# Kernel optimization log

Measured on AMD Instinct MI355X. Metric: run time of the kernel, lower is better.

## Reference

```python
import jax, jax.numpy as jnp
import numpy as np

N_NODES = 100000
N_EDGES = 1600000
N_GRAPHS = 64
D_IN = 128
D_HID = 128
D_OUT = 4
LEAKY_SLOPE = 0.01  # nn.LeakyReLU default


def setup_inputs() -> dict:
    key = jax.random.key(0)
    k1, k2, k3, k4, k5 = jax.random.split(key, 5)
    x = jax.random.normal(k1, (N_NODES, D_IN), dtype=jnp.float32)
    edge_index = jax.random.randint(k2, (2, N_EDGES), 0, N_NODES, dtype=jnp.int32)
    batch = jnp.sort(jax.random.randint(k3, (N_NODES,), 0, N_GRAPHS, dtype=jnp.int32))
    s1 = 1.0 / np.sqrt(D_IN)
    W1 = jax.random.uniform(k4, (D_IN, D_HID), jnp.float32, -s1, s1)
    b1 = jnp.zeros((D_HID,), jnp.float32)
    W2 = jax.random.uniform(k5, (D_HID, D_OUT), jnp.float32, -s1, s1)
    b2 = jnp.zeros((D_OUT,), jnp.float32)
    return {"x": x, "edge_index": edge_index, "batch": batch,
            "W1": W1, "b1": b1, "W2": W2, "b2": b2}


def _gcn_conv(x, src, dst, norm, W, b, n_nodes):
    # h = X W; messages = norm * h[src]; aggregate at dst; add bias
    h = x @ W
    msg = h[src] * norm[:, None]
    agg = jax.ops.segment_sum(msg, dst, num_segments=n_nodes)
    return agg + b


def reference(x, edge_index, batch, W1, b1, W2, b2):
    n = x.shape[0]
    # add self-loops (PyG GCNConv default)
    loops = jnp.arange(n, dtype=edge_index.dtype)
    src = jnp.concatenate([edge_index[0], loops])
    dst = jnp.concatenate([edge_index[1], loops])
    # symmetric normalization: deg over target index, weight 1
    deg = jax.ops.segment_sum(jnp.ones_like(src, dtype=x.dtype), dst, num_segments=n)
    deg_is = jnp.where(deg > 0, jax.lax.rsqrt(deg), 0.0)
    norm = deg_is[src] * deg_is[dst]

    h = _gcn_conv(x, src, dst, norm, W1, b1, n)
    h = jnp.where(h >= 0, h, LEAKY_SLOPE * h)  # LeakyReLU
    # dropout is identity at inference
    h = _gcn_conv(h, src, dst, norm, W2, b2, n)

    # global mean pool over graphs
    sums = jax.ops.segment_sum(h, batch, num_segments=N_GRAPHS)
    cnts = jax.ops.segment_sum(jnp.ones((n,), h.dtype), batch, num_segments=N_GRAPHS)
    pooled = sums / jnp.maximum(cnts, 1.0)[:, None]
    return jax.nn.softmax(pooled, axis=1)
```

## Files before the change

kernel.cpp:

```cpp
#include <hip/hip_runtime.h>

#define D 128
#define NG 64
#define NPB 256
#define MAXBK 512
#define CAPB 8192
#define PCHUNK 4096
#define PLCAP 5376
#define ENTCAP 21
#define NPASS 4
#define LDA 136

typedef unsigned int uint;
typedef unsigned short ushort_t;
typedef unsigned char uchar_t;
typedef float v2f __attribute__((ext_vector_type(2)));
typedef short s8v __attribute__((ext_vector_type(8)));
typedef float f4v __attribute__((ext_vector_type(4)));

__device__ __forceinline__ uint bfr(float x) {
    uint u = __float_as_uint(x);
    return (u + 0x7FFFu + ((u >> 16) & 1u)) >> 16;
}

__global__ __launch_bounds__(256) void k_init(const float* __restrict__ W,
                                              short* __restrict__ W1T,
                                              int* __restrict__ gcur, int NBK) {
    int idx = blockIdx.x * 256 + threadIdx.x;
    int nn = idx >> 7, kk = idx & 127;
    W1T[idx] = (short)bfr(W[kk * D + nn]);
    if (idx < NBK) gcur[idx] = idx * CAPB;
}

__global__ __launch_bounds__(256) void k_part(const int* __restrict__ edge,
                                              int* __restrict__ gcur, int* __restrict__ p1,
                                              int E, int NBK) {
    __shared__ int hist[MAXBK], scn[MAXBK], curb[MAXBK], fixb[MAXBK];
    __shared__ int ps[256];
    __shared__ int sortb[PCHUNK];
    __shared__ ushort_t sbkt[PCHUNK];
    int tid = threadIdx.x;
    for (int i = tid; i < MAXBK; i += 256) { hist[i] = 0; curb[i] = 0; }
    __syncthreads();
    int lo = blockIdx.x * PCHUNK;
    int hi = min(lo + PCHUNK, E);
    int cnt = hi - lo;
    for (int e = lo + tid; e < hi; e += 256) atomicAdd(&hist[edge[E + e] >> 8], 1);
    __syncthreads();
    int a = hist[2 * tid], b = hist[2 * tid + 1];
    ps[tid] = a + b;
    __syncthreads();
    for (int o = 1; o < 256; o <<= 1) {
        int x = (tid >= o) ? ps[tid - o] : 0;
        __syncthreads();
        ps[tid] += x;
        __syncthreads();
    }
    int pe = ps[tid] - (a + b);
    scn[2 * tid] = pe;
    scn[2 * tid + 1] = pe + a;
    __syncthreads();
    for (int bk = tid; bk < NBK; bk += 256)
        if (hist[bk]) fixb[bk] = atomicAdd(&gcur[bk], hist[bk]) - scn[bk];
    __syncthreads();
    for (int e = lo + tid; e < hi; e += 256) {
        int s = edge[e];
        int d2 = edge[E + e];
        int bk = d2 >> 8;
        int r = scn[bk] + atomicAdd(&curb[bk], 1);
        sortb[r] = ((d2 & 255) << 17) | s;
        sbkt[r] = (ushort_t)bk;
    }
    __syncthreads();
    for (int p = tid; p < cnt; p += 256) {
        int bk = sbkt[p];
        p1[fixb[bk] + p] = sortb[p];
    }
}

__global__ __launch_bounds__(256) void k_place(const int* __restrict__ p1,
                                               const int* __restrict__ gcur,
                                               int* __restrict__ ed, int2* __restrict__ offdeg,
                                               float* __restrict__ dinv, int n) {
    __shared__ int cnts[256], scn[256], cur[256];
    __shared__ int outb[PLCAP];
    int tid = threadIdx.x;
    int b = blockIdx.x;
    int base = b * CAPB;
    int cnt = gcur[b] - base;
    int end = base + cnt;
    int node0 = b << 8;
    cnts[tid] = 0;
    cur[tid] = 0;
    __syncthreads();
    int ent[ENTCAP];
    int ne = 0;
    for (int p = base + tid; p < end; p += 256) {
        int v = p1[p];
        if (ne < ENTCAP) ent[ne] = v;
        ne++;
        atomicAdd(&cnts[v >> 17], 1);
    }
    __syncthreads();
    int v0 = cnts[tid];
    scn[tid] = v0;
    __syncthreads();
    for (int o = 1; o < 256; o <<= 1) {
        int x = (tid >= o) ? scn[tid - o] : 0;
        __syncthreads();
        scn[tid] += x;
        __syncthreads();
    }
    int excl = scn[tid] - v0;
    int node = node0 + tid;
    if (node < n) {
        offdeg[node] = make_int2(base + excl, v0);
        dinv[node] = rsqrtf((float)(v0 + 1));
    }
    scn[tid] = excl;
    __syncthreads();
    int m = (ne < ENTCAP) ? ne : ENTCAP;
    for (int k = 0; k < m; ++k) {
        int v = ent[k];
        int l = v >> 17;
        int r = scn[l] + atomicAdd(&cur[l], 1);
        if (r < PLCAP) outb[r] = v & 0x1FFFF;
        else ed[base + r] = v & 0x1FFFF;
    }
    for (int p = base + tid + ENTCAP * 256; p < end; p += 256) {
        int v = p1[p];
        int l = v >> 17;
        int r = scn[l] + atomicAdd(&cur[l], 1);
        if (r < PLCAP) outb[r] = v & 0x1FFFF;
        else ed[base + r] = v & 0x1FFFF;
    }
    __syncthreads();
    int lim = (cnt < PLCAP) ? cnt : PLCAP;
    for (int p = tid; p < lim; p += 256) ed[base + p] = outb[p];
}

__global__ __launch_bounds__(256) void k_gemm_mfma(const float* __restrict__ X,
                                                   const short* __restrict__ W1T,
                                                   const float* __restrict__ dinv,
                                                   uchar_t* __restrict__ H8b, int M) {
    __shared__ short sA[128 * LDA];
    __shared__ short sB[128 * LDA];
    __shared__ float sDinv[128];
    const int tid = threadIdx.x;
    const int blockM = blockIdx.x * 128;

    if (tid < 128) {
        int gm = blockM + tid;
        sDinv[tid] = (gm < M) ? dinv[gm] : 0.f;
    }
    {
        int c = tid & 31, g = tid >> 5;
#pragma unroll
        for (int i = 0; i < 16; ++i) {
            int r = g + i * 8;
            int gm = blockM + r;
            float4 v = make_float4(0, 0, 0, 0);
            if (gm < M) v = *(const float4*)&X[(size_t)gm * D + c * 4];
            uint lo = bfr(v.x) | (bfr(v.y) << 16);
            uint hi = bfr(v.z) | (bfr(v.w) << 16);
            *(uint2*)&sA[r * LDA + c * 4] = make_uint2(lo, hi);
        }
    }
    {
        int nn = tid >> 1, seg = tid & 1;
        const short* src = W1T + nn * 128 + seg * 64;
        short* dst = &sB[nn * LDA + seg * 64];
#pragma unroll
        for (int i = 0; i < 8; ++i)
            *(int4*)&dst[i * 8] = *(const int4*)&src[i * 8];
    }
    __syncthreads();

    const int wv = tid >> 6;
    const int lane = tid & 63;
    const int m0w = (wv >> 1) * 64, n0w = (wv & 1) * 64;
    const int mrow = lane & 15;
    const int quad = lane >> 4;

    f4v acc[4][4];
#pragma unroll
    for (int mi = 0; mi < 4; ++mi)
#pragma unroll
        for (int ni = 0; ni < 4; ++ni) acc[mi][ni] = (f4v)(0.f);

#pragma unroll
    for (int ks = 0; ks < 4; ++ks) {
        s8v af[4], bf[4];
#pragma unroll
        for (int mi = 0; mi < 4; ++mi)
            af[mi] = *(const s8v*)&sA[(m0w + mi * 16 + mrow) * LDA + ks * 32 + quad * 8];
#pragma unroll
        for (int ni = 0; ni < 4; ++ni)
            bf[ni] = *(const s8v*)&sB[(n0w + ni * 16 + mrow) * LDA + ks * 32 + quad * 8];
#pragma unroll
        for (int mi = 0; mi < 4; ++mi)
#pragma unroll
            for (int ni = 0; ni < 4; ++ni)
                acc[mi][ni] = __builtin_amdgcn_mfma_f32_16x16x32_bf16(af[mi], bf[ni], acc[mi][ni], 0, 0, 0);
    }

#pragma unroll
    for (int mi = 0; mi < 4; ++mi) {
#pragma unroll
        for (int r = 0; r < 4; ++r) {
            int lrow = m0w + mi * 16 + quad * 4 + r;
            int gm = blockM + lrow;
            if (gm >= M) continue;
            float di = sDinv[lrow];
#pragma unroll
            for (int ni = 0; ni < 4; ++ni) {
                int col = n0w + ni * 16 + mrow;
                float v = acc[mi][ni][r] * di;
                uint p = __builtin_amdgcn_cvt_pk_fp8_f32(v, v, 0u, false);
                H8b[((size_t)(col >> 5) * M + gm) * 32 + (col & 31)] = (uchar_t)(p & 0xFF);
            }
        }
    }
}

__global__ __launch_bounds__(256) void k_gather(const uint* __restrict__ Hsu,
                                                const int2* __restrict__ offdeg,
                                                const int* __restrict__ ed,
                                                const float* __restrict__ dinv,
                                                const float* __restrict__ b1,
                                                const float* __restrict__ W2,
                                                float4* __restrict__ zpart,
                                                int n) {
    __shared__ float sW[128];
    __shared__ float sb[32];
    int tid = threadIdx.x;
    int p = blockIdx.x & 3;
    if (tid < 128) sW[tid] = W2[p * 128 + tid];
    if (tid < 32) sb[tid] = b1[p * 32 + tid];
    __syncthreads();
    int node = (blockIdx.x >> 2) * 32 + (tid >> 3);
    if (node >= n) return;
    int lane = tid & 7;
    const uint* T = Hsu + (size_t)p * n * 8;
    float di = dinv[node];
    uint h0 = T[(node << 3) + lane];
    v2f lo = __builtin_amdgcn_cvt_pk_f32_fp8(h0, false);
    v2f hi = __builtin_amdgcn_cvt_pk_f32_fp8(h0, true);
    float acc0 = lo.x, acc1 = lo.y, acc2 = hi.x, acc3 = hi.y;
    int2 od = offdeg[node];
    int j0 = od.x, j1 = od.x + od.y;
    int j = j0;
    for (; j + 8 <= j1; j += 8) {
        uint r[8];
#pragma unroll
        for (int k = 0; k < 8; ++k) r[k] = T[(ed[j + k] << 3) + lane];
#pragma unroll
        for (int k = 0; k < 8; ++k) {
            v2f l2 = __builtin_amdgcn_cvt_pk_f32_fp8(r[k], false);
            v2f h2 = __builtin_amdgcn_cvt_pk_f32_fp8(r[k], true);
            acc0 += l2.x; acc1 += l2.y; acc2 += h2.x; acc3 += h2.y;
        }
    }
    for (; j < j1; ++j) {
        uint rr = T[(ed[j] << 3) + lane];
        v2f l2 = __builtin_amdgcn_cvt_pk_f32_fp8(rr, false);
        v2f h2 = __builtin_amdgcn_cvt_pk_f32_fp8(rr, true);
        acc0 += l2.x; acc1 += l2.y; acc2 += h2.x; acc3 += h2.y;
    }
    int f = lane * 4;
    float v0 = di * acc0 + sb[f + 0];
    float v1 = di * acc1 + sb[f + 1];
    float v2 = di * acc2 + sb[f + 2];
    float v3 = di * acc3 + sb[f + 3];
    v0 = v0 >= 0.f ? v0 : 0.01f * v0;
    v1 = v1 >= 0.f ? v1 : 0.01f * v1;
    v2 = v2 >= 0.f ? v2 : 0.01f * v2;
    v3 = v3 >= 0.f ? v3 : 0.01f * v3;
    float a0 = v0 * sW[f * 4 + 0] + v1 * sW[(f + 1) * 4 + 0] + v2 * sW[(f + 2) * 4 + 0] + v3 * sW[(f + 3) * 4 + 0];
    float a1 = v0 * sW[f * 4 + 1] + v1 * sW[(f + 1) * 4 + 1] + v2 * sW[(f + 2) * 4 + 1] + v3 * sW[(f + 3) * 4 + 1];
    float a2 = v0 * sW[f * 4 + 2] + v1 * sW[(f + 1) * 4 + 2] + v2 * sW[(f + 2) * 4 + 2] + v3 * sW[(f + 3) * 4 + 2];
    float a3 = v0 * sW[f * 4 + 3] + v1 * sW[(f + 1) * 4 + 3] + v2 * sW[(f + 2) * 4 + 3] + v3 * sW[(f + 3) * 4 + 3];
#pragma unroll
    for (int o = 4; o >= 1; o >>= 1) {
        a0 += __shfl_xor(a0, o);
        a1 += __shfl_xor(a1, o);
        a2 += __shfl_xor(a2, o);
        a3 += __shfl_xor(a3, o);
    }
    if (lane == 0) zpart[(size_t)p * n + node] = make_float4(a0, a1, a2, a3);
}

__global__ __launch_bounds__(256) void k_zred(const float4* __restrict__ zpart,
                                              const float* __restrict__ dinv,
                                              float4* __restrict__ zs,
                                              float* __restrict__ psum,
                                              float* __restrict__ pcnt, int n) {
    int tid = threadIdx.x;
    if (blockIdx.x == 0) {
        if (tid < NG * 4) psum[tid] = 0.f;
        if (tid < NG) pcnt[tid] = 0.f;
    }
    int i = blockIdx.x * 256 + tid;
    if (i >= n) return;
    float4 a = zpart[i];
    float4 b = zpart[(size_t)n + i];
    float4 c = zpart[(size_t)2 * n + i];
    float4 d = zpart[(size_t)3 * n + i];
    float di = dinv[i];
    zs[i] = make_float4(di * (a.x + b.x + c.x + d.x), di * (a.y + b.y + c.y + d.y),
                        di * (a.z + b.z + c.z + d.z), di * (a.w + b.w + c.w + d.w));
}

__global__ __launch_bounds__(256) void k_pool2(const int* __restrict__ p1,
                                               const int* __restrict__ gcur,
                                               const float4* __restrict__ zs,
                                               const float* __restrict__ dinv,
                                               const int* __restrict__ batch,
                                               float* __restrict__ psum, float* __restrict__ pcnt,
                                               int n) {
    __shared__ float ls[NG * 4];
    __shared__ float lc[NG];
    __shared__ float dinvd[NPB];
    __shared__ int gl[NPB];
    int tid = threadIdx.x;
    int b = blockIdx.x >> 1;
    int half = blockIdx.x & 1;
    int node0 = b << 8;
    int node = node0 + tid;
    ls[tid] = 0.f;
    if (tid < NG) lc[tid] = 0.f;
    bool valid = node < n;
    float di = valid ? dinv[node] : 0.f;
    int g = valid ? batch[node] : -1;
    dinvd[tid] = di;
    gl[tid] = g;
    __syncthreads();
    float a0 = 0.f, a1 = 0.f, a2 = 0.f, a3 = 0.f;
    int cg = -1;
    if (half == 0 && valid) {
        float4 zv = zs[node];
        cg = g;
        a0 = di * zv.x; a1 = di * zv.y; a2 = di * zv.z; a3 = di * zv.w;
        atomicAdd(&lc[g], 1.f);
    }
    int base = b * CAPB;
    int cnt = gcur[b] - base;
    int mid = cnt >> 1;
    int s0 = base + (half ? mid : 0);
    int s1 = base + (half ? cnt : mid);
    for (int p = s0 + tid; p < s1; p += 1024) {
        int vv[4];
        float4 zb[4];
        int nb = 0;
#pragma unroll
        for (int k = 0; k < 4; ++k) {
            int q = p + k * 256;
            if (q < s1) vv[nb++] = p1[q];
        }
#pragma unroll
        for (int k = 0; k < 4; ++k)
            if (k < nb) zb[k] = zs[vv[k] & 0x1FFFF];
#pragma unroll
        for (int k = 0; k < 4; ++k) {
            if (k >= nb) continue;
            int dl = vv[k] >> 17;
            float w = dinvd[dl];
            int eg = gl[dl];
            if (eg != cg) {
                if (cg >= 0) {
                    atomicAdd(&ls[cg * 4 + 0], a0);
                    atomicAdd(&ls[cg * 4 + 1], a1);
                    atomicAdd(&ls[cg * 4 + 2], a2);
                    atomicAdd(&ls[cg * 4 + 3], a3);
                }
                cg = eg;
                a0 = a1 = a2 = a3 = 0.f;
            }
            a0 += w * zb[k].x; a1 += w * zb[k].y; a2 += w * zb[k].z; a3 += w * zb[k].w;
        }
    }
    if (cg >= 0) {
        atomicAdd(&ls[cg * 4 + 0], a0);
        atomicAdd(&ls[cg * 4 + 1], a1);
        atomicAdd(&ls[cg * 4 + 2], a2);
        atomicAdd(&ls[cg * 4 + 3], a3);
    }
    __syncthreads();
    atomicAdd(&psum[tid], ls[tid]);
    if (tid < NG) atomicAdd(&pcnt[tid], lc[tid]);
}

__global__ void k_final(const float* __restrict__ psum, const float* __restrict__ pcnt,
                        const float* __restrict__ b2, float* __restrict__ out) {
    int g = threadIdx.x;
    float c = fmaxf(pcnt[g], 1.f);
    float inv = 1.f / c;
    float l0 = psum[g * 4 + 0] * inv + b2[0];
    float l1 = psum[g * 4 + 1] * inv + b2[1];
    float l2 = psum[g * 4 + 2] * inv + b2[2];
    float l3 = psum[g * 4 + 3] * inv + b2[3];
    float m = fmaxf(fmaxf(l0, l1), fmaxf(l2, l3));
    float e0 = expf(l0 - m), e1 = expf(l1 - m), e2 = expf(l2 - m), e3 = expf(l3 - m);
    float s = 1.f / (e0 + e1 + e2 + e3);
    *(float4*)&out[g * 4] = make_float4(e0 * s, e1 * s, e2 * s, e3 * s);
}

extern "C" void kernel_launch(void* const* d_in, const int* in_sizes, int n_in,
                              void* d_out, int out_size, void* d_ws, size_t ws_size,
                              hipStream_t stream) {
    const float* X = (const float*)d_in[0];
    const int* edge = (const int*)d_in[1];
    const int* batch = (const int*)d_in[2];
    const float* W1 = (const float*)d_in[3];
    const float* b1 = (const float*)d_in[4];
    const float* W2 = (const float*)d_in[5];
    const float* b2 = (const float*)d_in[6];
    float* out = (float*)d_out;
    const int n = in_sizes[2];
    const int E = in_sizes[1] / 2;
    const int NBK = (n + NPB - 1) / NPB;

    uint* Hs = (uint*)d_ws;
    int* p1 = (int*)(Hs + (size_t)n * 32);
    int* ed = p1 + (size_t)NBK * CAPB;
    float4* zpart = (float4*)(ed + (size_t)NBK * CAPB);
    float4* zs = zpart + (size_t)NPASS * n;
    float* dinv = (float*)(zs + n);
    int2* offdeg = (int2*)(dinv + n);
    short* W1T = (short*)(offdeg + n);
    int* gcur = (int*)(W1T + 16384);
    float* psum = (float*)(gcur + MAXBK);
    float* pcnt = psum + NG * 4;

    const int NP = (E + PCHUNK - 1) / PCHUNK;
    const int NGB = (n + 31) / 32;

    k_init<<<64, 256, 0, stream>>>(W1, W1T, gcur, NBK);
    k_part<<<NP, 256, 0, stream>>>(edge, gcur, p1, E, NBK);
    k_place<<<NBK, 256, 0, stream>>>(p1, gcur, ed, offdeg, dinv, n);

    k_gemm_mfma<<<(n + 127) / 128, 256, 0, stream>>>(X, W1T, dinv, (uchar_t*)Hs, n);

    k_gather<<<NGB * NPASS, 256, 0, stream>>>(Hs, offdeg, ed, dinv, b1, W2, zpart, n);
    k_zred<<<(n + 255) / 256, 256, 0, stream>>>(zpart, dinv, zs, psum, pcnt, n);

    k_pool2<<<NBK * 2, 256, 0, stream>>>(p1, gcur, zs, dinv, batch, psum, pcnt, n);
    k_final<<<1, 64, 0, stream>>>(psum, pcnt, b2, out);
}
```

Before: 242.0 us.

## Merge preprocessing and post-GEMM kernels into two cooperative persistent kernels

Replaces the init/partition/place kernels with one cooperative kernel that uses grid-wide syncs between phases. The gather, z-reduction, pooling and softmax kernels become a second cooperative kernel with grid-stride loops. The aim is to cut launch overhead and inter-kernel gaps across the eight small launches. In exchange, grid size is capped by occupancy, so each phase runs at reduced parallelism, and grid.sync itself has a cost.

Result: slower. 709.8 us (+193.4%).

```diff
diff --git a/kernel.cpp b/kernel.cpp
--- a/kernel.cpp
+++ b/kernel.cpp
@@ -1,4 +1,7 @@
 #include <hip/hip_runtime.h>
+#include <hip/hip_cooperative_groups.h>
+
+namespace cg = cooperative_groups;
 
 #define D 128
 #define NG 64
@@ -23,120 +26,140 @@
     return (u + 0x7FFFu + ((u >> 16) & 1u)) >> 16;
 }
 
-__global__ __launch_bounds__(256) void k_init(const float* __restrict__ W,
-                                              short* __restrict__ W1T,
-                                              int* __restrict__ gcur, int NBK) {
-    int idx = blockIdx.x * 256 + threadIdx.x;
-    int nn = idx >> 7, kk = idx & 127;
-    W1T[idx] = (short)bfr(W[kk * D + nn]);
-    if (idx < NBK) gcur[idx] = idx * CAPB;
-}
-
-__global__ __launch_bounds__(256) void k_part(const int* __restrict__ edge,
-                                              int* __restrict__ gcur, int* __restrict__ p1,
-                                              int E, int NBK) {
-    __shared__ int hist[MAXBK], scn[MAXBK], curb[MAXBK], fixb[MAXBK];
-    __shared__ int ps[256];
-    __shared__ int sortb[PCHUNK];
-    __shared__ ushort_t sbkt[PCHUNK];
+__global__ __launch_bounds__(256, 4) void k_mega1(
+        const float* __restrict__ W1, const int* __restrict__ edge,
+        short* __restrict__ W1T, int* __restrict__ gcur, int* __restrict__ p1,
+        int* __restrict__ ed, int2* __restrict__ offdeg, float* __restrict__ dinv,
+        float* __restrict__ psum, float* __restrict__ pcnt,
+        int n, int E, int NBK, int NP) {
+    cg::grid_group grid = cg::this_grid();
+    __shared__ __align__(16) char smem[33792];
     int tid = threadIdx.x;
-    for (int i = tid; i < MAXBK; i += 256) { hist[i] = 0; curb[i] = 0; }
-    __syncthreads();
-    int lo = blockIdx.x * PCHUNK;
-    int hi = min(lo + PCHUNK, E);
-    int cnt = hi - lo;
-    for (int e = lo + tid; e < hi; e += 256) atomicAdd(&hist[edge[E + e] >> 8], 1);
-    __syncthreads();
-    int a = hist[2 * tid], b = hist[2 * tid + 1];
-    ps[tid] = a + b;
-    __syncthreads();
-    for (int o = 1; o < 256; o <<= 1) {
-        int x = (tid >= o) ? ps[tid - o] : 0;
-        __syncthreads();
-        ps[tid] += x;
-        __syncthreads();
-    }
-    int pe = ps[tid] - (a + b);
-    scn[2 * tid] = pe;
-    scn[2 * tid + 1] = pe + a;
-    __syncthreads();
-    for (int bk = tid; bk < NBK; bk += 256)
-        if (hist[bk]) fixb[bk] = atomicAdd(&gcur[bk], hist[bk]) - scn[bk];
-    __syncthreads();
-    for (int e = lo + tid; e < hi; e += 256) {
-        int s = edge[e];
-        int d2 = edge[E + e];
-        int bk = d2 >> 8;
-        int r = scn[bk] + atomicAdd(&curb[bk], 1);
-        sortb[r] = ((d2 & 255) << 17) | s;
-        sbkt[r] = (ushort_t)bk;
-    }
-    __syncthreads();
-    for (int p = tid; p < cnt; p += 256) {
-        int bk = sbkt[p];
-        p1[fixb[bk] + p] = sortb[p];
-    }
-}
-
-__global__ __launch_bounds__(256) void k_place(const int* __restrict__ p1,
-                                               const int* __restrict__ gcur,
-                                               int* __restrict__ ed, int2* __restrict__ offdeg,
-                                               float* __restrict__ dinv, int n) {
-    __shared__ int cnts[256], scn[256], cur[256];
-    __shared__ int outb[PLCAP];
-    int tid = threadIdx.x;
-    int b = blockIdx.x;
-    int base = b * CAPB;
-    int cnt = gcur[b] - base;
-    int end = base + cnt;
-    int node0 = b << 8;
-    cnts[tid] = 0;
-    cur[tid] = 0;
-    __syncthreads();
-    int ent[ENTCAP];
-    int ne = 0;
-    for (int p = base + tid; p < end; p += 256) {
-        int v = p1[p];
-        if (ne < ENTCAP) ent[ne] = v;
-        ne++;
-        atomicAdd(&cnts[v >> 17], 1);
-    }
-    __syncthreads();
-    int v0 = cnts[tid];
-    scn[tid] = v0;
-    __syncthreads();
-    for (int o = 1; o < 256; o <<= 1) {
-        int x = (tid >= o) ? scn[tid - o] : 0;
-        __syncthreads();
-        scn[tid] += x;
-        __syncthreads();
-    }
-    int excl = scn[tid] - v0;
-    int node = node0 + tid;
-    if (node < n) {
-        offdeg[node] = make_int2(base + excl, v0);
-        dinv[node] = rsqrtf((float)(v0 + 1));
-    }
-    scn[tid] = excl;
-    __syncthreads();
-    int m = (ne < ENTCAP) ? ne : ENTCAP;
-    for (int k = 0; k < m; ++k) {
-        int v = ent[k];
-        int l = v >> 17;
-        int r = scn[l] + atomicAdd(&cur[l], 1);
-        if (r < PLCAP) outb[r] = v & 0x1FFFF;
-        else ed[base + r] = v & 0x1FFFF;
-    }
-    for (int p = base + tid + ENTCAP * 256; p < end; p += 256) {
-        int v = p1[p];
-        int l = v >> 17;
-        int r = scn[l] + atomicAdd(&cur[l], 1);
-        if (r < PLCAP) outb[r] = v & 0x1FFFF;
-        else ed[base + r] = v & 0x1FFFF;
-    }
-    __syncthreads();
-    int lim = (cnt < PLCAP) ? cnt : PLCAP;
-    for (int p = tid; p < lim; p += 256) ed[base + p] = outb[p];
+
+    {
+        int idx = blockIdx.x * 256 + tid;
+        if (idx < 16384) {
+            int nn = idx >> 7, kk = idx & 127;
+            W1T[idx] = (short)bfr(W1[kk * D + nn]);
+        }
+        if (blockIdx.x == 0) {
+            for (int i = tid; i < NBK; i += 256) gcur[i] = i * CAPB;
+            if (tid < NG * 4) psum[tid] = 0.f;
+            if (tid < NG) pcnt[tid] = 0.f;
+        }
+    }
+    grid.sync();
+
+    {
+        int* hist = (int*)smem;
+        int* scn = hist + MAXBK;
+        int* curb = scn + MAXBK;
+        int* fixb = curb + MAXBK;
+        int* ps = fixb + MAXBK;
+        int* sortb = ps + 256;
+        ushort_t* sbkt = (ushort_t*)(sortb + PCHUNK);
+        for (int blk = blockIdx.x; blk < NP; blk += gridDim.x) {
+            __syncthreads();
+            for (int i = tid; i < MAXBK; i += 256) { hist[i] = 0; curb[i] = 0; }
+            __syncthreads();
+            int lo = blk * PCHUNK;
+            int hi = min(lo + PCHUNK, E);
+            int cnt2 = hi - lo;
+            for (int e = lo + tid; e < hi; e += 256) atomicAdd(&hist[edge[E + e] >> 8], 1);
+            __syncthreads();
+            int a = hist[2 * tid], b = hist[2 * tid + 1];
+            ps[tid] = a + b;
+            __syncthreads();
+            for (int o = 1; o < 256; o <<= 1) {
+                int x = (tid >= o) ? ps[tid - o] : 0;
+                __syncthreads();
+                ps[tid] += x;
+                __syncthreads();
+            }
+            int pe = ps[tid] - (a + b);
+            scn[2 * tid] = pe;
+            scn[2 * tid + 1] = pe + a;
+            __syncthreads();
+            for (int bk = tid; bk < NBK; bk += 256)
+                if (hist[bk]) fixb[bk] = atomicAdd(&gcur[bk], hist[bk]) - scn[bk];
+            __syncthreads();
+            for (int e = lo + tid; e < hi; e += 256) {
+                int s = edge[e];
+                int d2 = edge[E + e];
+                int bk = d2 >> 8;
+                int r = scn[bk] + atomicAdd(&curb[bk], 1);
+                sortb[r] = ((d2 & 255) << 17) | s;
+                sbkt[r] = (ushort_t)bk;
+            }
+            __syncthreads();
+            for (int q = tid; q < cnt2; q += 256) {
+                int bk = sbkt[q];
+                p1[fixb[bk] + q] = sortb[q];
+            }
+        }
+    }
+    grid.sync();
+
+    {
+        int* cnts = (int*)smem;
+        int* scn = cnts + 256;
+        int* cur = scn + 256;
+        int* outb = cur + 256;
+        for (int b = blockIdx.x; b < NBK; b += gridDim.x) {
+            __syncthreads();
+            int base = b * CAPB;
+            int cnt = gcur[b] - base;
+            int end = base + cnt;
+            int node0 = b << 8;
+            cnts[tid] = 0;
+            cur[tid] = 0;
+            __syncthreads();
+            int ent[ENTCAP];
+            int ne = 0;
+            for (int q = base + tid; q < end; q += 256) {
+                int v = p1[q];
+                if (ne < ENTCAP) ent[ne] = v;
+                ne++;
+                atomicAdd(&cnts[v >> 17], 1);
+            }
+            __syncthreads();
+            int v0 = cnts[tid];
+            scn[tid] = v0;
+            __syncthreads();
+            for (int o = 1; o < 256; o <<= 1) {
+                int x = (tid >= o) ? scn[tid - o] : 0;
+                __syncthreads();
+                scn[tid] += x;
+                __syncthreads();
+            }
+            int excl = scn[tid] - v0;
+            int node = node0 + tid;
+            if (node < n) {
+                offdeg[node] = make_int2(base + excl, v0);
+                dinv[node] = rsqrtf((float)(v0 + 1));
+            }
+            scn[tid] = excl;
+            __syncthreads();
+            int m = (ne < ENTCAP) ? ne : ENTCAP;
+            for (int k = 0; k < m; ++k) {
+                int v = ent[k];
+                int l = v >> 17;
+                int r = scn[l] + atomicAdd(&cur[l], 1);
+                if (r < PLCAP) outb[r] = v & 0x1FFFF;
+                else ed[base + r] = v & 0x1FFFF;
+            }
+            for (int q = base + tid + ENTCAP * 256; q < end; q += 256) {
+                int v = p1[q];
+                int l = v >> 17;
+                int r = scn[l] + atomicAdd(&cur[l], 1);
+                if (r < PLCAP) outb[r] = v & 0x1FFFF;
+                else ed[base + r] = v & 0x1FFFF;
+            }
+            __syncthreads();
+            int lim = (cnt < PLCAP) ? cnt : PLCAP;
+            for (int q = tid; q < lim; q += 256) ed[base + q] = outb[q];
+        }
+    }
 }
 
 __global__ __launch_bounds__(256) void k_gemm_mfma(const float* __restrict__ X,
@@ -223,186 +246,182 @@
     }
 }
 
-__global__ __launch_bounds__(256) void k_gather(const uint* __restrict__ Hsu,
-                                                const int2* __restrict__ offdeg,
-                                                const int* __restrict__ ed,
-                                                const float* __restrict__ dinv,
-                                                const float* __restrict__ b1,
-                                                const float* __restrict__ W2,
-                                                float4* __restrict__ zpart,
-                                                int n) {
-    __shared__ float sW[128];
-    __shared__ float sb[32];
+__global__ __launch_bounds__(256, 8) void k_mega2(
+        const uint* __restrict__ Hsu, const int2* __restrict__ offdeg,
+        const int* __restrict__ ed, const float* __restrict__ dinv,
+        const float* __restrict__ b1, const float* __restrict__ W2,
+        const int* __restrict__ batch, const float* __restrict__ b2,
+        const int* __restrict__ p1, const int* __restrict__ gcur,
+        float4* __restrict__ zpart, float4* __restrict__ zs,
+        float* __restrict__ psum, float* __restrict__ pcnt, float* __restrict__ out,
+        int n, int NBK, int NCH) {
+    cg::grid_group grid = cg::this_grid();
+    __shared__ __align__(16) char smem[3584];
     int tid = threadIdx.x;
-    int p = blockIdx.x & 3;
-    if (tid < 128) sW[tid] = W2[p * 128 + tid];
-    if (tid < 32) sb[tid] = b1[p * 32 + tid];
-    __syncthreads();
-    int node = (blockIdx.x >> 2) * 32 + (tid >> 3);
-    if (node >= n) return;
-    int lane = tid & 7;
-    const uint* T = Hsu + (size_t)p * n * 8;
-    float di = dinv[node];
-    uint h0 = T[(node << 3) + lane];
-    v2f lo = __builtin_amdgcn_cvt_pk_f32_fp8(h0, false);
-    v2f hi = __builtin_amdgcn_cvt_pk_f32_fp8(h0, true);
-    float acc0 = lo.x, acc1 = lo.y, acc2 = hi.x, acc3 = hi.y;
-    int2 od = offdeg[node];
-    int j0 = od.x, j1 = od.x + od.y;
-    int j = j0;
-    for (; j + 8 <= j1; j += 8) {
-        uint r[8];
-#pragma unroll
-        for (int k = 0; k < 8; ++k) r[k] = T[(ed[j + k] << 3) + lane];
-#pragma unroll
-        for (int k = 0; k < 8; ++k) {
-            v2f l2 = __builtin_amdgcn_cvt_pk_f32_fp8(r[k], false);
-            v2f h2 = __builtin_amdgcn_cvt_pk_f32_fp8(r[k], true);
-            acc0 += l2.x; acc1 += l2.y; acc2 += h2.x; acc3 += h2.y;
-        }
-    }
-    for (; j < j1; ++j) {
-        uint rr = T[(ed[j] << 3) + lane];
-        v2f l2 = __builtin_amdgcn_cvt_pk_f32_fp8(rr, false);
-        v2f h2 = __builtin_amdgcn_cvt_pk_f32_fp8(rr, true);
-        acc0 += l2.x; acc1 += l2.y; acc2 += h2.x; acc3 += h2.y;
-    }
-    int f = lane * 4;
-    float v0 = di * acc0 + sb[f + 0];
-    float v1 = di * acc1 + sb[f + 1];
-    float v2 = di * acc2 + sb[f + 2];
-    float v3 = di * acc3 + sb[f + 3];
-    v0 = v0 >= 0.f ? v0 : 0.01f * v0;
-    v1 = v1 >= 0.f ? v1 : 0.01f * v1;
-    v2 = v2 >= 0.f ? v2 : 0.01f * v2;
-    v3 = v3 >= 0.f ? v3 : 0.01f * v3;
-    float a0 = v0 * sW[f * 4 + 0] + v1 * sW[(f + 1) * 4 + 0] + v2 * sW[(f + 2) * 4 + 0] + v3 * sW[(f + 3) * 4 + 0];
-    float a1 = v0 * sW[f * 4 + 1] + v1 * sW[(f + 1) * 4 + 1] + v2 * sW[(f + 2) * 4 + 1] + v3 * sW[(f + 3) * 4 + 1];
-    float a2 = v0 * sW[f * 4 + 2] + v1 * sW[(f + 1) * 4 + 2] + v2 * sW[(f + 2) * 4 + 2] + v3 * sW[(f + 3) * 4 + 2];
-    float a3 = v0 * sW[f * 4 + 3] + v1 * sW[(f + 1) * 4 + 3] + v2 * sW[(f + 2) * 4 + 3] + v3 * sW[(f + 3) * 4 + 3];
-#pragma unroll
-    for (int o = 4; o >= 1; o >>= 1) {
-        a0 += __shfl_xor(a0, o);
-        a1 += __shfl_xor(a1, o);
-        a2 += __shfl_xor(a2, o);
-        a3 += __shfl_xor(a3, o);
-    }
-    if (lane == 0) zpart[(size_t)p * n + node] = make_float4(a0, a1, a2, a3);
-}
-
-__global__ __launch_bounds__(256) void k_zred(const float4* __restrict__ zpart,
-                                              const float* __restrict__ dinv,
-                                              float4* __restrict__ zs,
-                                              float* __restrict__ psum,
-                                              float* __restrict__ pcnt, int n) {
-    int tid = threadIdx.x;
-    if (blockIdx.x == 0) {
-        if (tid < NG * 4) psum[tid] = 0.f;
-        if (tid < NG) pcnt[tid] = 0.f;
-    }
-    int i = blockIdx.x * 256 + tid;
-    if (i >= n) return;
-    float4 a = zpart[i];
-    float4 b = zpart[(size_t)n + i];
-    float4 c = zpart[(size_t)2 * n + i];
-    float4 d = zpart[(size_t)3 * n + i];
-    float di = dinv[i];
-    zs[i] = make_float4(di * (a.x + b.x + c.x + d.x), di * (a.y + b.y + c.y + d.y),
-                        di * (a.z + b.z + c.z + d.z), di * (a.w + b.w + c.w + d.w));
-}
-
-__global__ __launch_bounds__(256) void k_pool2(const int* __restrict__ p1,
-                                               const int* __restrict__ gcur,
-                                               const float4* __restrict__ zs,
-                                               const float* __restrict__ dinv,
-                                               const int* __restrict__ batch,
-                                               float* __restrict__ psum, float* __restrict__ pcnt,
-                                               int n) {
-    __shared__ float ls[NG * 4];
-    __shared__ float lc[NG];
-    __shared__ float dinvd[NPB];
-    __shared__ int gl[NPB];
-    int tid = threadIdx.x;
-    int b = blockIdx.x >> 1;
-    int half = blockIdx.x & 1;
-    int node0 = b << 8;
-    int node = node0 + tid;
-    ls[tid] = 0.f;
-    if (tid < NG) lc[tid] = 0.f;
-    bool valid = node < n;
-    float di = valid ? dinv[node] : 0.f;
-    int g = valid ? batch[node] : -1;
-    dinvd[tid] = di;
-    gl[tid] = g;
-    __syncthreads();
-    float a0 = 0.f, a1 = 0.f, a2 = 0.f, a3 = 0.f;
-    int cg = -1;
-    if (half == 0 && valid) {
-        float4 zv = zs[node];
-        cg = g;
-        a0 = di * zv.x; a1 = di * zv.y; a2 = di * zv.z; a3 = di * zv.w;
-        atomicAdd(&lc[g], 1.f);
-    }
-    int base = b * CAPB;
-    int cnt = gcur[b] - base;
-    int mid = cnt >> 1;
-    int s0 = base + (half ? mid : 0);
-    int s1 = base + (half ? cnt : mid);
-    for (int p = s0 + tid; p < s1; p += 1024) {
-        int vv[4];
-        float4 zb[4];
-        int nb = 0;
-#pragma unroll
-        for (int k = 0; k < 4; ++k) {
-            int q = p + k * 256;
-            if (q < s1) vv[nb++] = p1[q];
-        }
-#pragma unroll
-        for (int k = 0; k < 4; ++k)
-            if (k < nb) zb[k] = zs[vv[k] & 0x1FFFF];
-#pragma unroll
-        for (int k = 0; k < 4; ++k) {
-            if (k >= nb) continue;
-            int dl = vv[k] >> 17;
-            float w = dinvd[dl];
-            int eg = gl[dl];
-            if (eg != cg) {
-                if (cg >= 0) {
-                    atomicAdd(&ls[cg * 4 + 0], a0);
-                    atomicAdd(&ls[cg * 4 + 1], a1);
-                    atomicAdd(&ls[cg * 4 + 2], a2);
-                    atomicAdd(&ls[cg * 4 + 3], a3);
+
+    {
+        float* sW = (float*)smem;
+        float* sb = sW + 128;
+        int p = blockIdx.x & 3;
+        if (tid < 128) sW[tid] = W2[p * 128 + tid];
+        if (tid < 32) sb[tid] = b1[p * 32 + tid];
+        __syncthreads();
+        const uint* T = Hsu + (size_t)p * n * 8;
+        int lane = tid & 7;
+        int gstep = gridDim.x >> 2;
+        for (int c = blockIdx.x >> 2; c < NCH; c += gstep) {
+            int node = c * 32 + (tid >> 3);
+            if (node < n) {
+                float di = dinv[node];
+                uint h0 = T[(node << 3) + lane];
+                v2f lo = __builtin_amdgcn_cvt_pk_f32_fp8(h0, false);
+                v2f hi = __builtin_amdgcn_cvt_pk_f32_fp8(h0, true);
+                float acc0 = lo.x, acc1 = lo.y, acc2 = hi.x, acc3 = hi.y;
+                int2 od = offdeg[node];
+                int j0 = od.x, j1 = od.x + od.y;
+                int j = j0;
+                for (; j + 8 <= j1; j += 8) {
+                    uint r[8];
+#pragma unroll
+                    for (int k = 0; k < 8; ++k) r[k] = T[(ed[j + k] << 3) + lane];
+#pragma unroll
+                    for (int k = 0; k < 8; ++k) {
+                        v2f l2 = __builtin_amdgcn_cvt_pk_f32_fp8(r[k], false);
+                        v2f h2 = __builtin_amdgcn_cvt_pk_f32_fp8(r[k], true);
+                        acc0 += l2.x; acc1 += l2.y; acc2 += h2.x; acc3 += h2.y;
+                    }
                 }
-                cg = eg;
-                a0 = a1 = a2 = a3 = 0.f;
-            }
-            a0 += w * zb[k].x; a1 += w * zb[k].y; a2 += w * zb[k].z; a3 += w * zb[k].w;
-        }
-    }
-    if (cg >= 0) {
-        atomicAdd(&ls[cg * 4 + 0], a0);
-        atomicAdd(&ls[cg * 4 + 1], a1);
-        atomicAdd(&ls[cg * 4 + 2], a2);
-        atomicAdd(&ls[cg * 4 + 3], a3);
-    }
-    __syncthreads();
-    atomicAdd(&psum[tid], ls[tid]);
-    if (tid < NG) atomicAdd(&pcnt[tid], lc[tid]);
-}
-
-__global__ void k_final(const float* __restrict__ psum, const float* __restrict__ pcnt,
-                        const float* __restrict__ b2, float* __restrict__ out) {
-    int g = threadIdx.x;
-    float c = fmaxf(pcnt[g], 1.f);
-    float inv = 1.f / c;
-    float l0 = psum[g * 4 + 0] * inv + b2[0];
-    float l1 = psum[g * 4 + 1] * inv + b2[1];
-    float l2 = psum[g * 4 + 2] * inv + b2[2];
-    float l3 = psum[g * 4 + 3] * inv + b2[3];
-    float m = fmaxf(fmaxf(l0, l1), fmaxf(l2, l3));
-    float e0 = expf(l0 - m), e1 = expf(l1 - m), e2 = expf(l2 - m), e3 = expf(l3 - m);
-    float s = 1.f / (e0 + e1 + e2 + e3);
-    *(float4*)&out[g * 4] = make_float4(e0 * s, e1 * s, e2 * s, e3 * s);
+                for (; j < j1; ++j) {
+                    uint rr = T[(ed[j] << 3) + lane];
+                    v2f l2 = __builtin_amdgcn_cvt_pk_f32_fp8(rr, false);
+                    v2f h2 = __builtin_amdgcn_cvt_pk_f32_fp8(rr, true);
+                    acc0 += l2.x; acc1 += l2.y; acc2 += h2.x; acc3 += h2.y;
+                }
+                int f = lane * 4;
+                float v0 = di * acc0 + sb[f + 0];
+                float v1 = di * acc1 + sb[f + 1];
+                float v2 = di * acc2 + sb[f + 2];
+                float v3 = di * acc3 + sb[f + 3];
+                v0 = v0 >= 0.f ? v0 : 0.01f * v0;
+                v1 = v1 >= 0.f ? v1 : 0.01f * v1;
+                v2 = v2 >= 0.f ? v2 : 0.01f * v2;
+                v3 = v3 >= 0.f ? v3 : 0.01f * v3;
+                float a0 = v0 * sW[f * 4 + 0] + v1 * sW[(f + 1) * 4 + 0] + v2 * sW[(f + 2) * 4 + 0] + v3 * sW[(f + 3) * 4 + 0];
+                float a1 = v0 * sW[f * 4 + 1] + v1 * sW[(f + 1) * 4 + 1] + v2 * sW[(f + 2) * 4 + 1] + v3 * sW[(f + 3) * 4 + 1];
+                float a2 = v0 * sW[f * 4 + 2] + v1 * sW[(f + 1) * 4 + 2] + v2 * sW[(f + 2) * 4 + 2] + v3 * sW[(f + 3) * 4 + 2];
+                float a3 = v0 * sW[f * 4 + 3] + v1 * sW[(f + 1) * 4 + 3] + v2 * sW[(f + 2) * 4 + 3] + v3 * sW[(f + 3) * 4 + 3];
+#pragma unroll
+                for (int o = 4; o >= 1; o >>= 1) {
+                    a0 += __shfl_xor(a0, o);
+                    a1 += __shfl_xor(a1, o);
+                    a2 += __shfl_xor(a2, o);
+                    a3 += __shfl_xor(a3, o);
+                }
+                if (lane == 0) zpart[(size_t)p * n + node] = make_float4(a0, a1, a2, a3);
+            }
+        }
+    }
+    grid.sync();
+
+    for (int i = blockIdx.x * 256 + tid; i < n; i += gridDim.x * 256) {
+        float4 a = zpart[i];
+        float4 b = zpart[(size_t)n + i];
+        float4 c = zpart[(size_t)2 * n + i];
+        float4 d = zpart[(size_t)3 * n + i];
+        float di = dinv[i];
+        zs[i] = make_float4(di * (a.x + b.x + c.x + d.x), di * (a.y + b.y + c.y + d.y),
+                            di * (a.z + b.z + c.z + d.z), di * (a.w + b.w + c.w + d.w));
+    }
+    grid.sync();
+
+    {
+        float* ls = (float*)smem;
+        float* lc = ls + NG * 4;
+        float* dinvd = lc + NG;
+        int* gl = (int*)(dinvd + NPB);
+        ls[tid] = 0.f;
+        if (tid < NG) lc[tid] = 0.f;
+        for (int hb = blockIdx.x; hb < 2 * NBK; hb += gridDim.x) {
+            __syncthreads();
+            int b = hb >> 1, half = hb & 1;
+            int node0 = b << 8;
+            int node = node0 + tid;
+            bool valid = node < n;
+            float di = valid ? dinv[node] : 0.f;
+            int g = valid ? batch[node] : -1;
+            dinvd[tid] = di;
+            gl[tid] = g;
+            __syncthreads();
+            float a0 = 0.f, a1 = 0.f, a2 = 0.f, a3 = 0.f;
+            int curg = -1;
+            if (half == 0 && valid) {
+                float4 zv = zs[node];
+                curg = g;
+                a0 = di * zv.x; a1 = di * zv.y; a2 = di * zv.z; a3 = di * zv.w;
+                atomicAdd(&lc[g], 1.f);
+            }
+            int base = b * CAPB;
+            int cnt = gcur[b] - base;
+            int mid = cnt >> 1;
+            int s0 = base + (half ? mid : 0);
+            int s1 = base + (half ? cnt : mid);
+            for (int q = s0 + tid; q < s1; q += 1024) {
+                int vv[4];
+                float4 zb[4];
+                int nb = 0;
+#pragma unroll
+                for (int k = 0; k < 4; ++k) {
+                    int qq = q + k * 256;
+                    if (qq < s1) vv[nb++] = p1[qq];
+                }
+#pragma unroll
+                for (int k = 0; k < 4; ++k)
+                    if (k < nb) zb[k] = zs[vv[k] & 0x1FFFF];
+#pragma unroll
+                for (int k = 0; k < 4; ++k) {
+                    if (k >= nb) continue;
+                    int dl = vv[k] >> 17;
+                    float w = dinvd[dl];
+                    int eg = gl[dl];
+                    if (eg != curg) {
+                        if (curg >= 0) {
+                            atomicAdd(&ls[curg * 4 + 0], a0);
+                            atomicAdd(&ls[curg * 4 + 1], a1);
+                            atomicAdd(&ls[curg * 4 + 2], a2);
+                            atomicAdd(&ls[curg * 4 + 3], a3);
+                        }
+                        curg = eg;
+                        a0 = a1 = a2 = a3 = 0.f;
+                    }
+                    a0 += w * zb[k].x; a1 += w * zb[k].y; a2 += w * zb[k].z; a3 += w * zb[k].w;
+                }
+            }
+            if (curg >= 0) {
+                atomicAdd(&ls[curg * 4 + 0], a0);
+                atomicAdd(&ls[curg * 4 + 1], a1);
+                atomicAdd(&ls[curg * 4 + 2], a2);
+                atomicAdd(&ls[curg * 4 + 3], a3);
+            }
+        }
+        __syncthreads();
+        atomicAdd(&psum[tid], ls[tid]);
+        if (tid < NG) atomicAdd(&pcnt[tid], lc[tid]);
+    }
+    grid.sync();
+
+    if (blockIdx.x == 0 && tid < NG) {
+        int g = tid;
+        float c = fmaxf(pcnt[g], 1.f);
+        float inv = 1.f / c;
+        float l0 = psum[g * 4 + 0] * inv + b2[0];
+        float l1 = psum[g * 4 + 1] * inv + b2[1];
+        float l2 = psum[g * 4 + 2] * inv + b2[2];
+        float l3 = psum[g * 4 + 3] * inv + b2[3];
+        float m = fmaxf(fmaxf(l0, l1), fmaxf(l2, l3));
+        float e0 = expf(l0 - m), e1 = expf(l1 - m), e2 = expf(l2 - m), e3 = expf(l3 - m);
+        float s = 1.f / (e0 + e1 + e2 + e3);
+        *(float4*)&out[g * 4] = make_float4(e0 * s, e1 * s, e2 * s, e3 * s);
+    }
 }
 
 extern "C" void kernel_launch(void* const* d_in, const int* in_sizes, int n_in,
@@ -416,9 +435,11 @@
     const float* W2 = (const float*)d_in[5];
     const float* b2 = (const float*)d_in[6];
     float* out = (float*)d_out;
-    const int n = in_sizes[2];
-    const int E = in_sizes[1] / 2;
-    const int NBK = (n + NPB - 1) / NPB;
+    int n = in_sizes[2];
+    int E = in_sizes[1] / 2;
+    int NBK = (n + NPB - 1) / NPB;
+    int NP = (E + PCHUNK - 1) / PCHUNK;
+    int NCH = (n + 31) / 32;
 
     uint* Hs = (uint*)d_ws;
     int* p1 = (int*)(Hs + (size_t)n * 32);
@@ -432,18 +453,32 @@
     float* psum = (float*)(gcur + MAXBK);
     float* pcnt = psum + NG * 4;
 
-    const int NP = (E + PCHUNK - 1) / PCHUNK;
-    const int NGB = (n + 31) / 32;
-
-    k_init<<<64, 256, 0, stream>>>(W1, W1T, gcur, NBK);
-    k_part<<<NP, 256, 0, stream>>>(edge, gcur, p1, E, NBK);
-    k_place<<<NBK, 256, 0, stream>>>(p1, gcur, ed, offdeg, dinv, n);
+    int bpc1 = 0, bpc2 = 0;
+    hipOccupancyMaxActiveBlocksPerMultiprocessor(&bpc1, k_mega1, 256, 0);
+    hipOccupancyMaxActiveBlocksPerMultiprocessor(&bpc2, k_mega2, 256, 0);
+    if (bpc1 < 1) bpc1 = 1;
+    if (bpc2 < 1) bpc2 = 1;
+    int grid1 = bpc1 * 256;
+    if (grid1 > NP) grid1 = NP;
+    int grid2 = bpc2 * 256;
+    if (grid2 > 2048) grid2 = 2048;
+    grid2 &= ~7;
+    if (grid2 < 8) grid2 = 8;
+
+    {
+        void* args[] = {(void*)&W1, (void*)&edge, (void*)&W1T, (void*)&gcur, (void*)&p1,
+                        (void*)&ed, (void*)&offdeg, (void*)&dinv, (void*)&psum, (void*)&pcnt,
+                        (void*)&n, (void*)&E, (void*)&NBK, (void*)&NP};
+        hipLaunchCooperativeKernel((void*)k_mega1, dim3(grid1), dim3(256), args, 0, stream);
+    }
 
     k_gemm_mfma<<<(n + 127) / 128, 256, 0, stream>>>(X, W1T, dinv, (uchar_t*)Hs, n);
 
-    k_gather<<<NGB * NPASS, 256, 0, stream>>>(Hs, offdeg, ed, dinv, b1, W2, zpart, n);
-    k_zred<<<(n + 255) / 256, 256, 0, stream>>>(zpart, dinv, zs, psum, pcnt, n);
-
-    k_pool2<<<NBK * 2, 256, 0, stream>>>(p1, gcur, zs, dinv, batch, psum, pcnt, n);
-    k_final<<<1, 64, 0, stream>>>(psum, pcnt, b2, out);
+    {
+        void* args[] = {(void*)&Hs, (void*)&offdeg, (void*)&ed, (void*)&dinv, (void*)&b1,
+                        (void*)&W2, (void*)&batch, (void*)&b2, (void*)&p1, (void*)&gcur,
+                        (void*)&zpart, (void*)&zs, (void*)&psum, (void*)&pcnt, (void*)&out,
+                        (void*)&n, (void*)&NBK, (void*)&NCH};
+        hipLaunchCooperativeKernel((void*)k_mega2, dim3(grid2), dim3(256), args, 0, stream);
+    }
 }
```
